# Kernel tuning notes

Hardware: AMD Instinct MI355X
Metric: run time of the kernel (lower is better)

## Reference

```python
import jax, jax.numpy as jnp
import numpy as np

N, n, D1, D2 = 16, 1024, 64, 64


def setup_inputs() -> dict:
    key = jax.random.key(0)
    ks = jax.random.split(key, 17)
    f = lambda k, shape: jax.random.normal(k, shape, dtype=jnp.float32)
    return {
        "A": f(ks[0], (N, n, n)),
        "X": f(ks[1], (N, n, D1)),
        "coeffs": f(ks[2], (5,)),
        "wA1": f(ks[3], (1, D1)),
        "wA2": f(ks[4], (1, D1)),
        "w11": f(ks[5], (D2, D1)),
        "w12": f(ks[6], (D2, D1)),
        "w13": f(ks[7], (D2, 1)),
        "w14": f(ks[8], (D2, 1)),
        "w15": f(ks[9], (D2, 1)),
        "w16": f(ks[10], (D2, 1)),
        "w21": f(ks[11], (D2, D1)),
        "w22": f(ks[12], (D2, D1)),
        "w23": f(ks[13], (D2, 1)),
        "w24": f(ks[14], (D2, 1)),
        "w25": f(ks[15], (D2, 1)),
        "w26": f(ks[16], (D2, 1)),
    }


def reference(A, X, coeffs, wA1, wA2, w11, w12, w13, w14, w15, w16,
              w21, w22, w23, w24, w25, w26):
    nn_ = A.shape[-1]
    diag = jnp.diagonal(A, axis1=-2, axis2=-1)          # (N, n)
    mean_diag = diag.mean(-1)                            # (N,)
    rowmean = A.mean(-1)                                 # (N, n) mean over columns
    mean_all = rowmean.mean(-1)                          # (N,)
    mean_X = X.mean(1)                                   # (N, D1)

    p1 = X @ wA1[0]                                      # (N, n)   Linear(D1->1) per node
    p2 = mean_X @ wA2[0]                                 # (N,)     Linear(D1->1) on mean

    # adjacency transform: scalar-weighted A + scalar stats + symmetrized row stats
    A_t = (coeffs[0] * A
           + (coeffs[1] * mean_all + coeffs[2] * mean_diag + p2)[:, None, None]
           + coeffs[3] * (rowmean[:, None, :] + rowmean[:, :, None])
           + coeffs[4] * (diag[:, None, :] + diag[:, :, None])
           + p1[:, None, :] + p1[:, :, None])             # (N, n, n)

    def node_transform(w_x, w_mx, w_col, w_diag, w_mdiag, w_mall):
        per_graph = (mean_X @ w_mx.T                      # (N, D2)
                     + mean_diag[:, None] * w_mdiag[:, 0][None, :]
                     + mean_all[:, None] * w_mall[:, 0][None, :])
        return (jnp.einsum('bnd,ed->bne', X, w_x)         # (N, n, D2)
                + rowmean[:, :, None] * w_col[:, 0]
                + diag[:, :, None] * w_diag[:, 0]
                + per_graph[:, None, :])

    X1_t = node_transform(w11, w12, w13, w14, w15, w16)
    X2_t = node_transform(w21, w22, w23, w24, w25, w26)

    out = A_t @ X2_t / nn_ + X1_t                         # (N, n, D2)
    return (A_t, out)
```

## Files before the change

kernel.cpp:

```cpp
#include <hip/hip_runtime.h>
#include <hip/hip_bf16.h>

#define NGRAPH 16
#define NNODE 1024
#define DDIM 64

typedef __attribute__((ext_vector_type(8))) short bf16x8;
typedef __attribute__((ext_vector_type(4))) float f32x4;

#define OFF_ROWSUM 0
#define OFF_DIAG   16384
#define OFF_P1     32768
#define OFF_R      49152
#define OFF_CS     65536
#define OFF_S      73728
#define OFF_S2P    75840
#define OFF_R2P    92224
#define OFF_BASE0  110656
#define OFF_X2T    1159232

__device__ __forceinline__ unsigned short f2bf(float f) {
    unsigned int u = __float_as_uint(f);
    u = (u + 0x7fffu + ((u >> 16) & 1u)) >> 16;
    return (unsigned short)u;
}

__device__ __forceinline__ float wave_reduce(float v) {
    #pragma unroll
    for (int off = 32; off; off >>= 1) v += __shfl_down(v, off, 64);
    return v;
}

__global__ __launch_bounds__(256) void kA_stats(const float* __restrict__ A,
                                                const float* __restrict__ X,
                                                const float* __restrict__ wA1,
                                                float* __restrict__ rowsum,
                                                float* __restrict__ diagv,
                                                float* __restrict__ p1,
                                                float* __restrict__ colsum_part) {
    if (blockIdx.x < NGRAPH * NNODE / 4) {
        int row  = blockIdx.x * 4 + (threadIdx.x >> 6);
        int lane = threadIdx.x & 63;
        const float4* b4 = (const float4*)(A + (size_t)row * NNODE);
        float sum = 0.f;
        #pragma unroll
        for (int it = 0; it < 4; ++it) {
            float4 v = b4[lane + it * 64];
            sum += v.x + v.y + v.z + v.w;
        }
        sum = wave_reduce(sum);
        if (lane == 0) {
            rowsum[row] = sum;
            int i = row & (NNODE - 1);
            diagv[row] = ((const float*)b4)[i];
        }
    } else {
        int bid  = blockIdx.x - NGRAPH * NNODE / 4;
        int b    = bid >> 3;
        int blk  = bid & 7;
        int wv   = threadIdx.x >> 6;
        int lane = threadIdx.x & 63;
        float w = wA1[lane];
        float cs = 0.f;
        int row0 = blk * 128 + wv * 32;
        const float* Xb = X + (size_t)b * NNODE * DDIM;
        for (int rI = 0; rI < 32; ++rI) {
            int i = row0 + rI;
            float x = Xb[i * DDIM + lane];
            cs += x;
            float v = wave_reduce(x * w);
            if (lane == 0) p1[b * NNODE + i] = v;
        }
        __shared__ float csl[4][64];
        csl[wv][lane] = cs;
        __syncthreads();
        if (threadIdx.x < 64) {
            float t = csl[0][lane] + csl[1][lane] + csl[2][lane] + csl[3][lane];
            colsum_part[(b * 8 + blk) * 64 + lane] = t;
        }
    }
}

__global__ __launch_bounds__(256) void kB_nodes(const float* __restrict__ X,
                                                const float* __restrict__ coeffs,
                                                const float* __restrict__ wA2,
                                                const float* __restrict__ w11,
                                                const float* __restrict__ w12,
                                                const float* __restrict__ w13,
                                                const float* __restrict__ w14,
                                                const float* __restrict__ w15,
                                                const float* __restrict__ w16,
                                                const float* __restrict__ w21,
                                                const float* __restrict__ w22,
                                                const float* __restrict__ w23,
                                                const float* __restrict__ w24,
                                                const float* __restrict__ w25,
                                                const float* __restrict__ w26,
                                                const float* __restrict__ rowsum,
                                                const float* __restrict__ diagv,
                                                const float* __restrict__ colsum_part,
                                                const float* __restrict__ p1g,
                                                float* __restrict__ rws,
                                                float* __restrict__ base0,
                                                unsigned short* __restrict__ x2tg,
                                                float* __restrict__ S2part,
                                                float* __restrict__ R2part,
                                                float* __restrict__ sArr) {
    __shared__ float Xl[64][68];
    __shared__ float w1l[64][68];
    __shared__ float w2l[64][68];
    __shared__ unsigned short X2Tl[64][68];
    __shared__ float rm_l[64], dg_l[64], r_l[64];
    __shared__ float redS[4][64], redR[4][64];
    __shared__ float redA[4], redD[4];
    __shared__ float mxs[64], p2s;
    __shared__ float pg1_l[64], pg2_l[64];

    int b    = blockIdx.x >> 4;
    int tile = blockIdx.x & 15;
    int i0   = tile * 64;
    int tid  = threadIdx.x;
    int e    = tid & 63;
    int wv   = tid >> 6;

    const float* Xg = X + (size_t)b * (NNODE * DDIM) + (size_t)i0 * DDIM;
    #pragma unroll
    for (int it = 0; it < 4; ++it) {
        int g   = it * 256 + tid;
        int row = g >> 4;
        int c4  = (g & 15) << 2;
        float4 v  = ((const float4*)Xg)[g];
        *(float4*)&Xl[row][c4] = v;
        float4 v1 = ((const float4*)w11)[g];
        *(float4*)&w1l[row][c4] = v1;
        float4 v2 = ((const float4*)w21)[g];
        *(float4*)&w2l[row][c4] = v2;
    }

    float sa = 0.f, sd = 0.f;
    for (int i = tid; i < NNODE; i += 256) {
        sa += rowsum[b * NNODE + i];
        sd += diagv[b * NNODE + i];
    }
    sa = wave_reduce(sa); sd = wave_reduce(sd);
    if (e == 0) { redA[wv] = sa; redD[wv] = sd; }
    if (tid < 64) {
        float mx = 0.f;
        for (int k = 0; k < 8; ++k) mx += colsum_part[(b * 8 + k) * 64 + tid];
        mxs[tid] = mx * (1.f / (float)NNODE);
    }
    __syncthreads();
    float mean_all  = (redA[0] + redA[1] + redA[2] + redA[3]) * (1.f / ((float)NNODE * (float)NNODE));
    float mean_diag = (redD[0] + redD[1] + redD[2] + redD[3]) * (1.f / (float)NNODE);
    if (tid < 64) {
        float v = wave_reduce(mxs[tid] * wA2[tid]);
        if (tid == 0) p2s = v;
    }
    if (tid < 64) {
        float a1 = 0.f, a2 = 0.f;
        for (int d = 0; d < 64; ++d) {
            float m = mxs[d];
            a1 += m * w12[tid * 64 + d];
            a2 += m * w22[tid * 64 + d];
        }
        pg1_l[tid] = a1 + mean_diag * w15[tid] + mean_all * w16[tid];
        pg2_l[tid] = a2 + mean_diag * w25[tid] + mean_all * w26[tid];
    }
    float c3 = coeffs[3], c4c = coeffs[4];
    if (tid < 64) {
        float rs  = rowsum[b * NNODE + i0 + tid];
        float dgv = diagv[b * NNODE + i0 + tid];
        float rmv = rs * (1.f / (float)NNODE);
        rm_l[tid] = rmv;
        dg_l[tid] = dgv;
        float rv = c3 * rmv + c4c * dgv + p1g[b * NNODE + i0 + tid];
        r_l[tid] = rv;
        rws[b * NNODE + i0 + tid] = rv;
    }
    __syncthreads();
    if (tile == 0 && tid == 0)
        sArr[b] = coeffs[1] * mean_all + coeffs[2] * mean_diag + p2s;

    float w13e = w13[e], w14e = w14[e], w23e = w23[e], w24e = w24[e];
    float pg1e = pg1_l[e], pg2e = pg2_l[e];

    float acc1[16], acc2[16];
    #pragma unroll
    for (int t = 0; t < 16; ++t) { acc1[t] = 0.f; acc2[t] = 0.f; }

    for (int d0 = 0; d0 < 64; d0 += 4) {
        float4 w1v = *(const float4*)&w1l[e][d0];
        float4 w2v = *(const float4*)&w2l[e][d0];
        #pragma unroll
        for (int t = 0; t < 16; ++t) {
            int li = wv + 4 * t;
            float4 xv = *(const float4*)&Xl[li][d0];
            acc1[t] += xv.x * w1v.x + xv.y * w1v.y + xv.z * w1v.z + xv.w * w1v.w;
            acc2[t] += xv.x * w2v.x + xv.y * w2v.y + xv.z * w2v.z + xv.w * w2v.w;
        }
    }

    float s2acc = 0.f, r2acc = 0.f;
    #pragma unroll
    for (int t = 0; t < 16; ++t) {
        int li = wv + 4 * t;
        int i  = i0 + li;
        float rmv = rm_l[li], dgv = dg_l[li];
        float x2t = acc2[t] + rmv * w23e + dgv * w24e + pg2e;
        float b0  = acc1[t] + rmv * w13e + dgv * w14e + pg1e;
        base0[((size_t)(b * NNODE + i)) * 64 + e] = b0;
        X2Tl[e][li] = f2bf(x2t);
        s2acc += x2t;
        r2acc += r_l[li] * x2t;
    }
    redS[wv][e] = s2acc;
    redR[wv][e] = r2acc;
    __syncthreads();

    for (int k = 0; k < 16; ++k) {
        int ep = wv * 16 + k;
        unsigned short v = X2Tl[ep][e];
        x2tg[((size_t)(b * 64 + ep)) * NNODE + i0 + e] = v;
    }
    if (tid < 64) {
        float s2 = redS[0][tid] + redS[1][tid] + redS[2][tid] + redS[3][tid];
        float r2 = redR[0][tid] + redR[1][tid] + redR[2][tid] + redR[3][tid];
        S2part[(b * 16 + tile) * 64 + tid] = s2;
        R2part[(b * 16 + tile) * 64 + tid] = r2;
    }
}

__global__ __launch_bounds__(256) void kC_main(const float* __restrict__ A,
                                               const float* __restrict__ coeffs,
                                               const float* __restrict__ sArr,
                                               const float* __restrict__ rArr,
                                               const unsigned short* __restrict__ x2tg,
                                               const float* __restrict__ base0,
                                               const float* __restrict__ S2part,
                                               const float* __restrict__ R2part,
                                               float* __restrict__ At,
                                               float* __restrict__ outp) {
    __shared__ unsigned short Al[2][16][136];
    __shared__ float r_lds[1024];
    __shared__ float s2_lds[64], r2_lds[64];

    int b    = blockIdx.x >> 6;
    int tile = blockIdx.x & 63;
    int i0   = tile * 16;
    int tid  = threadIdx.x;

    float4 rv = ((const float4*)(rArr + b * NNODE))[tid];
    *(float4*)&r_lds[tid * 4] = rv;
    if (tid < 64) {
        float s2 = 0.f, r2 = 0.f;
        #pragma unroll
        for (int t = 0; t < 16; ++t) {
            s2 += S2part[(b * 16 + t) * 64 + tid];
            r2 += R2part[(b * 16 + t) * 64 + tid];
        }
        s2_lds[tid] = s2 * (1.f / (float)NNODE);
        r2_lds[tid] = r2 * (1.f / (float)NNODE);
    }

    float sb  = sArr[b];
    float c0  = coeffs[0];
    float c0n = c0 * (1.f / (float)NNODE);

    int arow = tid >> 4;
    int acol = (tid & 15) * 8;
    const float* Ab  = A  + ((size_t)(b * NNODE + i0 + arow)) * NNODE + acol;
    float*       Atb = At + ((size_t)(b * NNODE + i0 + arow)) * NNODE + acol;

    int lane = tid & 63, wv = tid >> 6;
    int m = lane & 15, quad = lane >> 4;
    int e = wv * 16 + m;
    const unsigned short* Bg = x2tg + ((size_t)(b * 64 + e)) * NNODE + quad * 8;

    f32x4 acc = {0.f, 0.f, 0.f, 0.f};

    __syncthreads();

    for (int kt = 0; kt < 8; ++kt) {
        bf16x8 bf0 = *(const bf16x8*)(Bg + kt * 128);
        bf16x8 bf1 = *(const bf16x8*)(Bg + kt * 128 + 32);
        bf16x8 bf2 = *(const bf16x8*)(Bg + kt * 128 + 64);
        bf16x8 bf3 = *(const bf16x8*)(Bg + kt * 128 + 96);

        float4 a0 = *(const float4*)(Ab + kt * 128);
        float4 a1 = *(const float4*)(Ab + kt * 128 + 4);
        float  ri = r_lds[i0 + arow];
        int cidx = kt * 128 + acol;
        float4 rj0 = *(const float4*)&r_lds[cidx];
        float4 rj1 = *(const float4*)&r_lds[cidx + 4];
        float bse = sb + ri;
        float4 t0, t1;
        t0.x = c0 * a0.x + bse + rj0.x; t0.y = c0 * a0.y + bse + rj0.y;
        t0.z = c0 * a0.z + bse + rj0.z; t0.w = c0 * a0.w + bse + rj0.w;
        t1.x = c0 * a1.x + bse + rj1.x; t1.y = c0 * a1.y + bse + rj1.y;
        t1.z = c0 * a1.z + bse + rj1.z; t1.w = c0 * a1.w + bse + rj1.w;
        *(float4*)(Atb + kt * 128)     = t0;
        *(float4*)(Atb + kt * 128 + 4) = t1;

        unsigned int p0 = (unsigned int)f2bf(a0.x) | ((unsigned int)f2bf(a0.y) << 16);
        unsigned int p1 = (unsigned int)f2bf(a0.z) | ((unsigned int)f2bf(a0.w) << 16);
        unsigned int p2 = (unsigned int)f2bf(a1.x) | ((unsigned int)f2bf(a1.y) << 16);
        unsigned int p3 = (unsigned int)f2bf(a1.z) | ((unsigned int)f2bf(a1.w) << 16);
        uint4 pk = {p0, p1, p2, p3};
        *(uint4*)&Al[kt & 1][arow][acol] = pk;

        __syncthreads();

        bf16x8 av0 = *(const bf16x8*)&Al[kt & 1][m][quad * 8];
        bf16x8 av1 = *(const bf16x8*)&Al[kt & 1][m][32 + quad * 8];
        bf16x8 av2 = *(const bf16x8*)&Al[kt & 1][m][64 + quad * 8];
        bf16x8 av3 = *(const bf16x8*)&Al[kt & 1][m][96 + quad * 8];
        acc = __builtin_amdgcn_mfma_f32_16x16x32_bf16(av0, bf0, acc, 0, 0, 0);
        acc = __builtin_amdgcn_mfma_f32_16x16x32_bf16(av1, bf1, acc, 0, 0, 0);
        acc = __builtin_amdgcn_mfma_f32_16x16x32_bf16(av2, bf2, acc, 0, 0, 0);
        acc = __builtin_amdgcn_mfma_f32_16x16x32_bf16(av3, bf3, acc, 0, 0, 0);
    }

    float s2 = s2_lds[e];
    float r2 = r2_lds[e];
    #pragma unroll
    for (int reg = 0; reg < 4; ++reg) {
        int i = i0 + quad * 4 + reg;
        float v = acc[reg] * c0n
                + base0[((size_t)(b * NNODE + i)) * 64 + e]
                + (sb + r_lds[i]) * s2 + r2;
        outp[((size_t)(b * NNODE + i)) * 64 + e] = v;
    }
}

extern "C" void kernel_launch(void* const* d_in, const int* in_sizes, int n_in,
                              void* d_out, int out_size, void* d_ws, size_t ws_size,
                              hipStream_t stream) {
    const float* A      = (const float*)d_in[0];
    const float* X      = (const float*)d_in[1];
    const float* coeffs = (const float*)d_in[2];
    const float* wA1    = (const float*)d_in[3];
    const float* wA2    = (const float*)d_in[4];
    const float* w11    = (const float*)d_in[5];
    const float* w12    = (const float*)d_in[6];
    const float* w13    = (const float*)d_in[7];
    const float* w14    = (const float*)d_in[8];
    const float* w15    = (const float*)d_in[9];
    const float* w16    = (const float*)d_in[10];
    const float* w21    = (const float*)d_in[11];
    const float* w22    = (const float*)d_in[12];
    const float* w23    = (const float*)d_in[13];
    const float* w24    = (const float*)d_in[14];
    const float* w25    = (const float*)d_in[15];
    const float* w26    = (const float*)d_in[16];

    float* ws  = (float*)d_ws;
    float* At  = (float*)d_out;
    float* out = (float*)d_out + (size_t)NGRAPH * NNODE * NNODE;

    float* rowsum = ws + OFF_ROWSUM;
    float* diagv  = ws + OFF_DIAG;
    float* p1     = ws + OFF_P1;
    float* rws    = ws + OFF_R;
    float* cspart = ws + OFF_CS;
    float* sArr   = ws + OFF_S;
    float* S2part = ws + OFF_S2P;
    float* R2part = ws + OFF_R2P;
    float* base0  = ws + OFF_BASE0;
    unsigned short* x2tg = (unsigned short*)(ws + OFF_X2T);

    kA_stats<<<NGRAPH * NNODE / 4 + NGRAPH * 8, 256, 0, stream>>>(
        A, X, wA1, rowsum, diagv, p1, cspart);
    kB_nodes<<<NGRAPH * 16, 256, 0, stream>>>(
        X, coeffs, wA2, w11, w12, w13, w14, w15, w16,
        w21, w22, w23, w24, w25, w26,
        rowsum, diagv, cspart, p1,
        rws, base0, x2tg, S2part, R2part, sArr);
    kC_main<<<NGRAPH * 64, 256, 0, stream>>>(
        A, coeffs, sArr, rws, x2tg, base0, S2part, R2part, At, out);
}
```

Baseline: 204.3 us.

## Load A fragments directly per wave, drop LDS staging and barriers

Each wave now reads its own A row slices from global memory and converts them to bf16 in registers for the MFMA, instead of staging a bf16 copy of A in LDS and synchronising every k-step. Each A element is therefore loaded by all four waves (rotated k-slices, one wave writes At), which quadruples global/L2 reads of A in exchange for removing per-iteration barriers and LDS traffic. Launch bounds now request 4 blocks per CU. The cost is redundant HBM/L2 reads of the largest tensor.

```diff
diff --git a/kernel.cpp b/kernel.cpp
--- a/kernel.cpp
+++ b/kernel.cpp
@@ -230,7 +230,7 @@
     }
 }
 
-__global__ __launch_bounds__(256) void kC_main(const float* __restrict__ A,
+__global__ __launch_bounds__(256, 4) void kC_main(const float* __restrict__ A,
                                                const float* __restrict__ coeffs,
                                                const float* __restrict__ sArr,
                                                const float* __restrict__ rArr,
@@ -240,7 +240,6 @@
                                                const float* __restrict__ R2part,
                                                float* __restrict__ At,
                                                float* __restrict__ outp) {
-    __shared__ unsigned short Al[2][16][136];
     __shared__ float r_lds[1024];
     __shared__ float s2_lds[64], r2_lds[64];
 
@@ -262,62 +261,58 @@
         r2_lds[tid] = r2 * (1.f / (float)NNODE);
     }
 
+    int lane = tid & 63, wv = tid >> 6;
+    int m = lane & 15, quad = lane >> 4;
+    int e = wv * 16 + m;
+    int qo = quad * 8;
+
+    const float* Arow            = A    + ((size_t)(b * NNODE + i0 + m)) * NNODE;
+    float*       Atrow           = At   + ((size_t)(b * NNODE + i0 + m)) * NNODE;
+    const unsigned short* Bg     = x2tg + ((size_t)(b * 64 + e)) * NNODE;
+
     float sb  = sArr[b];
     float c0  = coeffs[0];
     float c0n = c0 * (1.f / (float)NNODE);
 
-    int arow = tid >> 4;
-    int acol = (tid & 15) * 8;
-    const float* Ab  = A  + ((size_t)(b * NNODE + i0 + arow)) * NNODE + acol;
-    float*       Atb = At + ((size_t)(b * NNODE + i0 + arow)) * NNODE + acol;
-
-    int lane = tid & 63, wv = tid >> 6;
-    int m = lane & 15, quad = lane >> 4;
-    int e = wv * 16 + m;
-    const unsigned short* Bg = x2tg + ((size_t)(b * 64 + e)) * NNODE + quad * 8;
+    __syncthreads();
+
+    float bse = sb + r_lds[i0 + m];
 
     f32x4 acc = {0.f, 0.f, 0.f, 0.f};
 
-    __syncthreads();
-
     for (int kt = 0; kt < 8; ++kt) {
-        bf16x8 bf0 = *(const bf16x8*)(Bg + kt * 128);
-        bf16x8 bf1 = *(const bf16x8*)(Bg + kt * 128 + 32);
-        bf16x8 bf2 = *(const bf16x8*)(Bg + kt * 128 + 64);
-        bf16x8 bf3 = *(const bf16x8*)(Bg + kt * 128 + 96);
-
-        float4 a0 = *(const float4*)(Ab + kt * 128);
-        float4 a1 = *(const float4*)(Ab + kt * 128 + 4);
-        float  ri = r_lds[i0 + arow];
-        int cidx = kt * 128 + acol;
-        float4 rj0 = *(const float4*)&r_lds[cidx];
-        float4 rj1 = *(const float4*)&r_lds[cidx + 4];
-        float bse = sb + ri;
-        float4 t0, t1;
-        t0.x = c0 * a0.x + bse + rj0.x; t0.y = c0 * a0.y + bse + rj0.y;
-        t0.z = c0 * a0.z + bse + rj0.z; t0.w = c0 * a0.w + bse + rj0.w;
-        t1.x = c0 * a1.x + bse + rj1.x; t1.y = c0 * a1.y + bse + rj1.y;
-        t1.z = c0 * a1.z + bse + rj1.z; t1.w = c0 * a1.w + bse + rj1.w;
-        *(float4*)(Atb + kt * 128)     = t0;
-        *(float4*)(Atb + kt * 128 + 4) = t1;
-
-        unsigned int p0 = (unsigned int)f2bf(a0.x) | ((unsigned int)f2bf(a0.y) << 16);
-        unsigned int p1 = (unsigned int)f2bf(a0.z) | ((unsigned int)f2bf(a0.w) << 16);
-        unsigned int p2 = (unsigned int)f2bf(a1.x) | ((unsigned int)f2bf(a1.y) << 16);
-        unsigned int p3 = (unsigned int)f2bf(a1.z) | ((unsigned int)f2bf(a1.w) << 16);
-        uint4 pk = {p0, p1, p2, p3};
-        *(uint4*)&Al[kt & 1][arow][acol] = pk;
-
-        __syncthreads();
-
-        bf16x8 av0 = *(const bf16x8*)&Al[kt & 1][m][quad * 8];
-        bf16x8 av1 = *(const bf16x8*)&Al[kt & 1][m][32 + quad * 8];
-        bf16x8 av2 = *(const bf16x8*)&Al[kt & 1][m][64 + quad * 8];
-        bf16x8 av3 = *(const bf16x8*)&Al[kt & 1][m][96 + quad * 8];
-        acc = __builtin_amdgcn_mfma_f32_16x16x32_bf16(av0, bf0, acc, 0, 0, 0);
-        acc = __builtin_amdgcn_mfma_f32_16x16x32_bf16(av1, bf1, acc, 0, 0, 0);
-        acc = __builtin_amdgcn_mfma_f32_16x16x32_bf16(av2, bf2, acc, 0, 0, 0);
-        acc = __builtin_amdgcn_mfma_f32_16x16x32_bf16(av3, bf3, acc, 0, 0, 0);
+        int k0 = kt * 128;
+        #pragma unroll
+        for (int j = 0; j < 4; ++j) {
+            int ks = (wv + j) & 3;
+            int c  = k0 + ks * 32 + qo;
+            float4 a0 = *(const float4*)(Arow + c);
+            float4 a1 = *(const float4*)(Arow + c + 4);
+            bf16x8 bv = *(const bf16x8*)(Bg + c);
+
+            if (j == 0) {
+                float4 rj0 = *(const float4*)&r_lds[c];
+                float4 rj1 = *(const float4*)&r_lds[c + 4];
+                f32x4 t0, t1;
+                t0.x = fmaf(c0, a0.x, bse + rj0.x);
+                t0.y = fmaf(c0, a0.y, bse + rj0.y);
+                t0.z = fmaf(c0, a0.z, bse + rj0.z);
+                t0.w = fmaf(c0, a0.w, bse + rj0.w);
+                t1.x = fmaf(c0, a1.x, bse + rj1.x);
+                t1.y = fmaf(c0, a1.y, bse + rj1.y);
+                t1.z = fmaf(c0, a1.z, bse + rj1.z);
+                t1.w = fmaf(c0, a1.w, bse + rj1.w);
+                *(f32x4*)(Atrow + c)     = t0;
+                *(f32x4*)(Atrow + c + 4) = t1;
+            }
+
+            union { uint4 u; bf16x8 v; } cvt;
+            cvt.u.x = (unsigned int)f2bf(a0.x) | ((unsigned int)f2bf(a0.y) << 16);
+            cvt.u.y = (unsigned int)f2bf(a0.z) | ((unsigned int)f2bf(a0.w) << 16);
+            cvt.u.z = (unsigned int)f2bf(a1.x) | ((unsigned int)f2bf(a1.y) << 16);
+            cvt.u.w = (unsigned int)f2bf(a1.z) | ((unsigned int)f2bf(a1.w) << 16);
+            acc = __builtin_amdgcn_mfma_f32_16x16x32_bf16(cvt.v, bv, acc, 0, 0, 0);
+        }
     }
 
     float s2 = s2_lds[e];
```

Result: slower. 222.3 us (+8.8%).

## Prefetch next A tile across barrier and use lighter LDS-only barrier

Applied to the files above, without the earlier changes.

Software-pipelines the global loads of A so the next k-tile's float4s are issued before the barrier, and replaces __syncthreads with an inline s_waitcnt lgkmcnt(0)+s_barrier that does not wait on outstanding global loads. It also hoists the row-bias computation out of the loop, uses fmaf, and changes the LDS row padding from 136 to 132. The goal is to hide global-load latency behind the MFMA work; the custom barrier depends on the compiler placing vmcnt waits correctly, and the new padding may change LDS bank conflicts.

```diff
diff --git a/kernel.cpp b/kernel.cpp
--- a/kernel.cpp
+++ b/kernel.cpp
@@ -240,7 +240,7 @@
                                                const float* __restrict__ R2part,
                                                float* __restrict__ At,
                                                float* __restrict__ outp) {
-    __shared__ unsigned short Al[2][16][136];
+    __shared__ unsigned short Al[2][16][132];
     __shared__ float r_lds[1024];
     __shared__ float s2_lds[64], r2_lds[64];
 
@@ -276,9 +276,14 @@
     int e = wv * 16 + m;
     const unsigned short* Bg = x2tg + ((size_t)(b * 64 + e)) * NNODE + quad * 8;
 
+    float4 a0 = *(const float4*)(Ab);
+    float4 a1 = *(const float4*)(Ab + 4);
+
     f32x4 acc = {0.f, 0.f, 0.f, 0.f};
 
     __syncthreads();
+
+    float bse = sb + r_lds[i0 + arow];
 
     for (int kt = 0; kt < 8; ++kt) {
         bf16x8 bf0 = *(const bf16x8*)(Bg + kt * 128);
@@ -286,29 +291,34 @@
         bf16x8 bf2 = *(const bf16x8*)(Bg + kt * 128 + 64);
         bf16x8 bf3 = *(const bf16x8*)(Bg + kt * 128 + 96);
 
-        float4 a0 = *(const float4*)(Ab + kt * 128);
-        float4 a1 = *(const float4*)(Ab + kt * 128 + 4);
-        float  ri = r_lds[i0 + arow];
         int cidx = kt * 128 + acol;
         float4 rj0 = *(const float4*)&r_lds[cidx];
         float4 rj1 = *(const float4*)&r_lds[cidx + 4];
-        float bse = sb + ri;
-        float4 t0, t1;
-        t0.x = c0 * a0.x + bse + rj0.x; t0.y = c0 * a0.y + bse + rj0.y;
-        t0.z = c0 * a0.z + bse + rj0.z; t0.w = c0 * a0.w + bse + rj0.w;
-        t1.x = c0 * a1.x + bse + rj1.x; t1.y = c0 * a1.y + bse + rj1.y;
-        t1.z = c0 * a1.z + bse + rj1.z; t1.w = c0 * a1.w + bse + rj1.w;
-        *(float4*)(Atb + kt * 128)     = t0;
-        *(float4*)(Atb + kt * 128 + 4) = t1;
-
-        unsigned int p0 = (unsigned int)f2bf(a0.x) | ((unsigned int)f2bf(a0.y) << 16);
-        unsigned int p1 = (unsigned int)f2bf(a0.z) | ((unsigned int)f2bf(a0.w) << 16);
-        unsigned int p2 = (unsigned int)f2bf(a1.x) | ((unsigned int)f2bf(a1.y) << 16);
-        unsigned int p3 = (unsigned int)f2bf(a1.z) | ((unsigned int)f2bf(a1.w) << 16);
-        uint4 pk = {p0, p1, p2, p3};
+        f32x4 t0, t1;
+        t0.x = fmaf(c0, a0.x, bse + rj0.x);
+        t0.y = fmaf(c0, a0.y, bse + rj0.y);
+        t0.z = fmaf(c0, a0.z, bse + rj0.z);
+        t0.w = fmaf(c0, a0.w, bse + rj0.w);
+        t1.x = fmaf(c0, a1.x, bse + rj1.x);
+        t1.y = fmaf(c0, a1.y, bse + rj1.y);
+        t1.z = fmaf(c0, a1.z, bse + rj1.z);
+        t1.w = fmaf(c0, a1.w, bse + rj1.w);
+        *(f32x4*)(Atb + kt * 128)     = t0;
+        *(f32x4*)(Atb + kt * 128 + 4) = t1;
+
+        uint4 pk;
+        pk.x = (unsigned int)f2bf(a0.x) | ((unsigned int)f2bf(a0.y) << 16);
+        pk.y = (unsigned int)f2bf(a0.z) | ((unsigned int)f2bf(a0.w) << 16);
+        pk.z = (unsigned int)f2bf(a1.x) | ((unsigned int)f2bf(a1.y) << 16);
+        pk.w = (unsigned int)f2bf(a1.z) | ((unsigned int)f2bf(a1.w) << 16);
         *(uint4*)&Al[kt & 1][arow][acol] = pk;
 
-        __syncthreads();
+        if (kt < 7) {
+            a0 = *(const float4*)(Ab + (kt + 1) * 128);
+            a1 = *(const float4*)(Ab + (kt + 1) * 128 + 4);
+        }
+
+        asm volatile("s_waitcnt lgkmcnt(0)\n\ts_barrier" ::: "memory");
 
         bf16x8 av0 = *(const bf16x8*)&Al[kt & 1][m][quad * 8];
         bf16x8 av1 = *(const bf16x8*)&Al[kt & 1][m][32 + quad * 8];
```

Measured after the change: 202.5 us. About the same (-0.9%).
